# Kernel optimization log

Hardware: AMD Instinct MI355X
Metric: run time of the kernel (lower is better)

The kernel has to match this reference:

```python
import jax, jax.numpy as jnp
import numpy as np


def _next_pow2(n: int) -> int:
    return 1 << (max(int(n), 1) - 1).bit_length()


def setup_inputs() -> dict:
    key = jax.random.key(0)
    k1, k2 = jax.random.split(key)
    B, L, D, K = 8, 8192, 256, 8192
    u = jax.random.normal(k1, (B, L, D), dtype=jnp.float32)
    h = jax.random.normal(k2, (D, K), dtype=jnp.float32) * 0.02  # RandomNormal(stddev=0.02)
    return {"u": u, "h": h}


def reference(u, h):
    # Depthwise long conv via zero-padded FFT, 'same' padding.
    # Faithful to the TF code, including its h-row pairing via tf.repeat:
    # x row i (= b*D + d) is multiplied by filter row i // B.
    u = u.astype(jnp.float32)
    B, L, D = u.shape
    K = h.shape[1]
    N = _next_pow2(L + K - 1)

    x = jnp.transpose(u, (0, 2, 1)).reshape(B * D, L)      # (B*D, L)
    x_pad = jnp.pad(x, ((0, 0), (0, N - L)))               # (B*D, N)
    h_pad = jnp.pad(h, ((0, 0), (0, N - K)))               # (D, N)

    X = jnp.fft.rfft(x_pad, axis=-1)                       # (B*D, N//2+1)
    H = jnp.fft.rfft(h_pad, axis=-1)                       # (D, N//2+1)
    # tf.repeat(h, B, axis=0): repeated row i corresponds to filter i // B
    row_filter = jnp.arange(B * D) // B                    # (B*D,)
    Y = X * H[row_filter]

    y_full = jnp.fft.irfft(Y, n=N, axis=-1)                # (B*D, N)
    start = (K - 1) // 2
    y = y_full[:, start:start + L]                         # (B*D, L)
    y = y.reshape(B, D, L)
    return jnp.transpose(y, (0, 2, 1))                     # (B, L, D)
```

## Files before the change

### kernel.cpp

```cpp
#include <hip/hip_runtime.h>

#define TPB 1024

__device__ constexpr int PX(int p) { return p + 2 * (p >> 5); }

#define LDS_F2 17408
#define LDS_BYTES (LDS_F2 * 8)

#define PIF 3.14159265358979323846f
#define C8 0.92387953251128674f
#define S8 0.38268343236508978f

struct Tw { float c1,s1,c2,s2,c3,s3; };

__device__ __forceinline__ Tw tw_make(float c1, float s1) {
  Tw w;
  w.c1 = c1; w.s1 = s1;
  w.c2 = c1*c1 - s1*s1;      w.s2 = 2.f*c1*s1;
  w.c3 = c1*w.c2 - s1*w.s2;  w.s3 = c1*w.s2 + s1*w.c2;
  return w;
}
__device__ __forceinline__ Tw tw_angle(float a) {
  float s, c; __sincosf(a, &s, &c); return tw_make(c, s);
}

__device__ __forceinline__ void r4dif(float2&a,float2&b,float2&c,float2&d,const Tw&w){
  float t0r=a.x+c.x, t0i=a.y+c.y, t1r=a.x-c.x, t1i=a.y-c.y;
  float t2r=b.x+d.x, t2i=b.y+d.y, t3r=b.x-d.x, t3i=b.y-d.y;
  float u0r=t0r+t2r, u0i=t0i+t2i, u2r=t0r-t2r, u2i=t0i-t2i;
  float u1r=t1r+t3i, u1i=t1i-t3r, u3r=t1r-t3i, u3i=t1i+t3r;
  a = make_float2(u0r, u0i);
  b = make_float2(u1r*w.c1 - u1i*w.s1, u1r*w.s1 + u1i*w.c1);
  c = make_float2(u2r*w.c2 - u2i*w.s2, u2r*w.s2 + u2i*w.c2);
  d = make_float2(u3r*w.c3 - u3i*w.s3, u3r*w.s3 + u3i*w.c3);
}
__device__ __forceinline__ void r4dif_z(float2&a,float2&b,float2&c,float2&d,const Tw&w){
  float u0r=a.x+b.x, u0i=a.y+b.y, u2r=a.x-b.x, u2i=a.y-b.y;
  float u1r=a.x+b.y, u1i=a.y-b.x, u3r=a.x-b.y, u3i=a.y+b.x;
  a = make_float2(u0r, u0i);
  b = make_float2(u1r*w.c1 - u1i*w.s1, u1r*w.s1 + u1i*w.c1);
  c = make_float2(u2r*w.c2 - u2i*w.s2, u2r*w.s2 + u2i*w.c2);
  d = make_float2(u3r*w.c3 - u3i*w.s3, u3r*w.s3 + u3i*w.c3);
}
__device__ __forceinline__ void r4dif_nt(float2&a,float2&b,float2&c,float2&d){
  float t0r=a.x+c.x, t0i=a.y+c.y, t1r=a.x-c.x, t1i=a.y-c.y;
  float t2r=b.x+d.x, t2i=b.y+d.y, t3r=b.x-d.x, t3i=b.y-d.y;
  a = make_float2(t0r+t2r, t0i+t2i);
  b = make_float2(t1r+t3i, t1i-t3r);
  c = make_float2(t0r-t2r, t0i-t2i);
  d = make_float2(t1r-t3i, t1i+t3r);
}
__device__ __forceinline__ void r4dit(float2&a,float2&b,float2&c,float2&d,const Tw&w){
  float v1r=b.x*w.c1 - b.y*w.s1, v1i=b.x*w.s1 + b.y*w.c1;
  float v2r=c.x*w.c2 - c.y*w.s2, v2i=c.x*w.s2 + c.y*w.c2;
  float v3r=d.x*w.c3 - d.y*w.s3, v3i=d.x*w.s3 + d.y*w.c3;
  float ar=a.x, ai=a.y;
  a = make_float2(ar+v1r+v2r+v3r, ai+v1i+v2i+v3i);
  b = make_float2(ar-v1i-v2r+v3i, ai+v1r-v2i-v3r);
  c = make_float2(ar-v1r+v2r-v3r, ai-v1i+v2i-v3i);
  d = make_float2(ar+v1i-v2r-v3i, ai-v1r-v2i+v3r);
}
__device__ __forceinline__ void r4dit_nt(float2&a,float2&b,float2&c,float2&d){
  float v1r=b.x, v1i=b.y, v2r=c.x, v2i=c.y, v3r=d.x, v3i=d.y;
  float ar=a.x, ai=a.y;
  a = make_float2(ar+v1r+v2r+v3r, ai+v1i+v2i+v3i);
  b = make_float2(ar-v1i-v2r+v3i, ai+v1r-v2i-v3r);
  c = make_float2(ar-v1r+v2r-v3r, ai-v1i+v2i-v3i);
  d = make_float2(ar+v1i-v2r-v3i, ai-v1r-v2i+v3r);
}

__device__ __forceinline__ void r16_fwd(float2 (&e)[16], float aA, float aB) {
  float c1, s1; __sincosf(aA, &s1, &c1);
#pragma unroll
  for (int r = 0; r < 4; ++r) {
    if (r) { float t = c1*C8 + s1*S8; s1 = s1*C8 - c1*S8; c1 = t; }
    Tw w = tw_make(c1, s1);
    r4dif(e[r], e[r+4], e[r+8], e[r+12], w);
  }
  Tw wb = tw_angle(aB);
#pragma unroll
  for (int m = 0; m < 4; ++m) r4dif(e[4*m], e[4*m+1], e[4*m+2], e[4*m+3], wb);
}
__device__ __forceinline__ void r16_fwd_z(float2 (&e)[16], float aA, float aB) {
  float c1, s1; __sincosf(aA, &s1, &c1);
#pragma unroll
  for (int r = 0; r < 4; ++r) {
    if (r) { float t = c1*C8 + s1*S8; s1 = s1*C8 - c1*S8; c1 = t; }
    Tw w = tw_make(c1, s1);
    r4dif_z(e[r], e[r+4], e[r+8], e[r+12], w);
  }
  Tw wb = tw_angle(aB);
#pragma unroll
  for (int m = 0; m < 4; ++m) r4dif(e[4*m], e[4*m+1], e[4*m+2], e[4*m+3], wb);
}
__device__ __forceinline__ void r16_inv(float2 (&e)[16], float aA, float aB) {
  Tw wa = tw_angle(aA);
#pragma unroll
  for (int j = 0; j < 4; ++j) r4dit(e[4*j], e[4*j+1], e[4*j+2], e[4*j+3], wa);
  float c1, s1; __sincosf(aB, &s1, &c1);
#pragma unroll
  for (int q = 0; q < 4; ++q) {
    if (q) { float t = c1*C8 - s1*S8; s1 = s1*C8 + c1*S8; c1 = t; }
    Tw w = tw_make(c1, s1);
    r4dit(e[q], e[q+4], e[q+8], e[q+12], w);
  }
}

__device__ __forceinline__ void fwd_mid(float2* A, int tid) {
  __syncthreads();
  {
    const int c = tid & 63;
    const int pb = PX(((tid >> 6) << 10) | c);
    float2 e[16];
#pragma unroll
    for (int k = 0; k < 16; ++k) e[k] = A[pb + PX(64*k)];
    r16_fwd(e, (float)c * (-PIF/512.f), (float)c * (-PIF/128.f));
#pragma unroll
    for (int k = 0; k < 16; ++k) A[pb + PX(64*k)] = e[k];
  }
  __syncthreads();
  {
    const int c = tid & 3;
    const int pb = PX(((tid >> 2) << 6) | c);
    float2 e[16];
#pragma unroll
    for (int k = 0; k < 16; ++k) e[k] = A[pb + PX(4*k)];
    r16_fwd(e, (float)c * (-PIF/32.f), (float)c * (-PIF/8.f));
#pragma unroll
    for (int k = 0; k < 16; ++k) A[pb + PX(4*k)] = e[k];
  }
  __syncthreads();
}

__global__ __launch_bounds__(TPB) void h_fft(const float* __restrict__ h,
                                             float2* __restrict__ Hbuf) {
  extern __shared__ __align__(16) float2 A[];
  const int tid = threadIdx.x;
  const int f = blockIdx.x;
  const float* hr = h + (size_t)f * 8192;
  float2 e[16];
#pragma unroll
  for (int k = 0; k < 8; ++k) e[k] = make_float2(hr[tid + 1024*k], 0.f);
  r16_fwd_z(e, (float)tid * (-PIF/8192.f), (float)tid * (-PIF/2048.f));
  const int pt = PX(tid);
#pragma unroll
  for (int k = 0; k < 16; ++k) A[pt + PX(1024*k)] = e[k];
  fwd_mid(A, tid);
  const float sc = 1.f / 16384.f;
  float2* orow = Hbuf + (size_t)f * 16384;
  const int p4 = PX(4*tid);
#pragma unroll
  for (int m = 0; m < 4; ++m) {
    const int pp = p4 + PX(4096*m);
    float4 lo = *(const float4*)&A[pp];
    float4 hi = *(const float4*)&A[pp+2];
    float2 a = make_float2(lo.x, lo.y), b = make_float2(lo.z, lo.w);
    float2 c = make_float2(hi.x, hi.y), d = make_float2(hi.z, hi.w);
    r4dif_nt(a, b, c, d);
    const int p = 4*tid + 4096*m;
    *(float4*)&orow[p]   = make_float4(a.x*sc, a.y*sc, b.x*sc, b.y*sc);
    *(float4*)&orow[p+2] = make_float4(c.x*sc, c.y*sc, d.x*sc, d.y*sc);
  }
}

__global__ __launch_bounds__(256) void transpose_in(const float* __restrict__ u,
                                                    float* __restrict__ xT) {
  __shared__ float T[64][65];
  const int l0 = blockIdx.x * 64, d0 = blockIdx.y * 64, b = blockIdx.z;
  const int t = threadIdx.x, c = t & 15, r = t >> 4;
  const float4* u4 = (const float4*)(u + (size_t)b * 8192 * 256);
#pragma unroll
  for (int p = 0; p < 4; ++p) {
    int li = r + 16 * p;
    float4 v = u4[(size_t)(l0 + li) * 64 + (d0 >> 2) + c];
    T[4*c+0][li] = v.x; T[4*c+1][li] = v.y; T[4*c+2][li] = v.z; T[4*c+3][li] = v.w;
  }
  __syncthreads();
#pragma unroll
  for (int p = 0; p < 4; ++p) {
    int dr = r + 16 * p;
    float4 w = make_float4(T[dr][4*c+0], T[dr][4*c+1], T[dr][4*c+2], T[dr][4*c+3]);
    *(float4*)&xT[(size_t)(b * 256 + d0 + dr) * 8192 + l0 + 4 * c] = w;
  }
}

__global__ __launch_bounds__(256) void transpose_out(const float* __restrict__ yT,
                                                     float* __restrict__ out) {
  __shared__ float T[64][65];
  const int l0 = blockIdx.x * 64, d0 = blockIdx.y * 64, b = blockIdx.z;
  const int t = threadIdx.x, c = t & 15, r = t >> 4;
#pragma unroll
  for (int p = 0; p < 4; ++p) {
    int di = r + 16 * p;
    float4 v = *(const float4*)&yT[(size_t)(b * 256 + d0 + di) * 8192 + l0 + 4 * c];
    T[4*c+0][di] = v.x; T[4*c+1][di] = v.y; T[4*c+2][di] = v.z; T[4*c+3][di] = v.w;
  }
  __syncthreads();
#pragma unroll
  for (int p = 0; p < 4; ++p) {
    int lr = r + 16 * p;
    float4 w = make_float4(T[lr][4*c+0], T[lr][4*c+1], T[lr][4*c+2], T[lr][4*c+3]);
    *(float4*)&out[(size_t)(b * 8192 + l0 + lr) * 256 + d0 + 4 * c] = w;
  }
}

__global__ __launch_bounds__(TPB) void conv_main(const float* __restrict__ xT,
                                                 const float2* __restrict__ Hbuf,
                                                 float* yT) {
  extern __shared__ __align__(16) float2 A[];
  const int tid = threadIdx.x;
  const int i = blockIdx.x;
  const int f = ((i >> 5) << 3) | (i & 7);
  const int r = (f << 3) | (((i >> 3) & 3) << 1);
  const float* x0 = xT + (size_t)r * 8192;
  const float* x1 = xT + (size_t)(r + 1) * 8192;

  float2 e[16];
#pragma unroll
  for (int k = 0; k < 8; ++k)
    e[k] = make_float2(x0[tid + 1024*k], x1[tid + 1024*k]);
  const float2* Hrow = Hbuf + (size_t)f * 16384;
  float4 hpre[8];
#pragma unroll
  for (int m = 0; m < 4; ++m) {
    hpre[2*m]   = *(const float4*)&Hrow[4*tid + 4096*m];
    hpre[2*m+1] = *(const float4*)&Hrow[4*tid + 4096*m + 2];
  }
  r16_fwd_z(e, (float)tid * (-PIF/8192.f), (float)tid * (-PIF/2048.f));
  const int pt = PX(tid);
#pragma unroll
  for (int k = 0; k < 16; ++k) A[pt + PX(1024*k)] = e[k];

  fwd_mid(A, tid);

  {
    const int p4 = PX(4*tid);
#pragma unroll
    for (int m = 0; m < 4; ++m) {
      const int pp = p4 + PX(4096*m);
      float4 lo = *(const float4*)&A[pp];
      float4 hi = *(const float4*)&A[pp+2];
      float2 a = make_float2(lo.x, lo.y), b = make_float2(lo.z, lo.w);
      float2 c = make_float2(hi.x, hi.y), d = make_float2(hi.z, hi.w);
      r4dif_nt(a, b, c, d);
      float4 h0 = hpre[2*m];
      float4 h1 = hpre[2*m+1];
      float2 an = make_float2(a.x*h0.x - a.y*h0.y, a.x*h0.y + a.y*h0.x);
      float2 bn = make_float2(b.x*h0.z - b.y*h0.w, b.x*h0.w + b.y*h0.z);
      float2 cn = make_float2(c.x*h1.x - c.y*h1.y, c.x*h1.y + c.y*h1.x);
      float2 dn = make_float2(d.x*h1.z - d.y*h1.w, d.x*h1.w + d.y*h1.z);
      r4dit_nt(an, bn, cn, dn);
      *(float4*)&A[pp]   = make_float4(an.x, an.y, bn.x, bn.y);
      *(float4*)&A[pp+2] = make_float4(cn.x, cn.y, dn.x, dn.y);
    }
  }
  __syncthreads();

  {
    const int c = tid & 3;
    const int pb = PX(((tid >> 2) << 6) | c);
#pragma unroll
    for (int k = 0; k < 16; ++k) e[k] = A[pb + PX(4*k)];
    r16_inv(e, (float)c * (PIF/8.f), (float)c * (PIF/32.f));
#pragma unroll
    for (int k = 0; k < 16; ++k) A[pb + PX(4*k)] = e[k];
  }
  __syncthreads();

  {
    const int c = tid & 63;
    const int pb = PX(((tid >> 6) << 10) | c);
#pragma unroll
    for (int k = 0; k < 16; ++k) e[k] = A[pb + PX(64*k)];
    r16_inv(e, (float)c * (PIF/128.f), (float)c * (PIF/512.f));
#pragma unroll
    for (int k = 0; k < 16; ++k) A[pb + PX(64*k)] = e[k];
  }
  __syncthreads();

  {
#pragma unroll
    for (int k = 0; k < 16; ++k) e[k] = A[pt + PX(1024*k)];
    r16_inv(e, (float)tid * (PIF/2048.f), (float)tid * (PIF/8192.f));
    float* y0 = yT + (size_t)r * 8192;
    float* y1 = yT + (size_t)(r + 1) * 8192;
#pragma unroll
    for (int k = 4; k <= 10; ++k) {
      const int l = tid + 1024*k - 4095;
      y0[l] = e[k].x; y1[l] = e[k].y;
    }
    if (tid < 1023) { const int l = tid + 1024*11 - 4095; y0[l] = e[11].x; y1[l] = e[11].y; }
    else            { y0[0] = e[3].x;  y1[0] = e[3].y; }
  }
}

extern "C" void kernel_launch(void* const* d_in, const int* in_sizes, int n_in,
                              void* d_out, int out_size, void* d_ws, size_t ws_size,
                              hipStream_t stream) {
  (void)in_sizes; (void)n_in; (void)out_size; (void)ws_size;
  const float* u = (const float*)d_in[0];
  const float* h = (const float*)d_in[1];
  float* out = (float*)d_out;
  float* xT = (float*)d_ws;
  float2* Hbuf = (float2*)((char*)d_ws + (size_t)2048 * 8192 * 4);

  static_assert(LDS_BYTES == 139264, "lds");
  (void)hipFuncSetAttribute((const void*)h_fft,
      hipFuncAttributeMaxDynamicSharedMemorySize, LDS_BYTES);
  (void)hipFuncSetAttribute((const void*)conv_main,
      hipFuncAttributeMaxDynamicSharedMemorySize, LDS_BYTES);

  h_fft<<<256, TPB, LDS_BYTES, stream>>>(h, Hbuf);
  transpose_in<<<dim3(128, 4, 8), 256, 0, stream>>>(u, xT);
  conv_main<<<1024, TPB, LDS_BYTES, stream>>>(xT, Hbuf, xT);
  transpose_out<<<dim3(128, 4, 8), 256, 0, stream>>>(xT, out);
}
```

Before: 248.3 us.

## Fuse input/output transposes into the FFT convolution kernel

Removes the separate transpose_in and transpose_out kernels and the intermediate transposed workspace. conv_main now reads two adjacent channels directly from u with a stride of 256 floats, and writes float2 results directly into out. The H spectrum loads move from an up-front register prefetch to just before the pointwise multiply. This eliminates two kernel launches and a full extra round trip of the activations through global memory, at the cost of strided, poorly coalesced global accesses that rely on cache reuse across blocks.

```diff
diff --git a/kernel.cpp b/kernel.cpp
--- a/kernel.cpp
+++ b/kernel.cpp
@@ -163,69 +163,23 @@
   }
 }
 
-__global__ __launch_bounds__(256) void transpose_in(const float* __restrict__ u,
-                                                    float* __restrict__ xT) {
-  __shared__ float T[64][65];
-  const int l0 = blockIdx.x * 64, d0 = blockIdx.y * 64, b = blockIdx.z;
-  const int t = threadIdx.x, c = t & 15, r = t >> 4;
-  const float4* u4 = (const float4*)(u + (size_t)b * 8192 * 256);
-#pragma unroll
-  for (int p = 0; p < 4; ++p) {
-    int li = r + 16 * p;
-    float4 v = u4[(size_t)(l0 + li) * 64 + (d0 >> 2) + c];
-    T[4*c+0][li] = v.x; T[4*c+1][li] = v.y; T[4*c+2][li] = v.z; T[4*c+3][li] = v.w;
-  }
-  __syncthreads();
-#pragma unroll
-  for (int p = 0; p < 4; ++p) {
-    int dr = r + 16 * p;
-    float4 w = make_float4(T[dr][4*c+0], T[dr][4*c+1], T[dr][4*c+2], T[dr][4*c+3]);
-    *(float4*)&xT[(size_t)(b * 256 + d0 + dr) * 8192 + l0 + 4 * c] = w;
-  }
-}
-
-__global__ __launch_bounds__(256) void transpose_out(const float* __restrict__ yT,
-                                                     float* __restrict__ out) {
-  __shared__ float T[64][65];
-  const int l0 = blockIdx.x * 64, d0 = blockIdx.y * 64, b = blockIdx.z;
-  const int t = threadIdx.x, c = t & 15, r = t >> 4;
-#pragma unroll
-  for (int p = 0; p < 4; ++p) {
-    int di = r + 16 * p;
-    float4 v = *(const float4*)&yT[(size_t)(b * 256 + d0 + di) * 8192 + l0 + 4 * c];
-    T[4*c+0][di] = v.x; T[4*c+1][di] = v.y; T[4*c+2][di] = v.z; T[4*c+3][di] = v.w;
-  }
-  __syncthreads();
-#pragma unroll
-  for (int p = 0; p < 4; ++p) {
-    int lr = r + 16 * p;
-    float4 w = make_float4(T[lr][4*c+0], T[lr][4*c+1], T[lr][4*c+2], T[lr][4*c+3]);
-    *(float4*)&out[(size_t)(b * 8192 + l0 + lr) * 256 + d0 + 4 * c] = w;
-  }
-}
-
-__global__ __launch_bounds__(TPB) void conv_main(const float* __restrict__ xT,
+__global__ __launch_bounds__(TPB) void conv_main(const float* __restrict__ u,
                                                  const float2* __restrict__ Hbuf,
-                                                 float* yT) {
+                                                 float* __restrict__ out) {
   extern __shared__ __align__(16) float2 A[];
   const int tid = threadIdx.x;
   const int i = blockIdx.x;
-  const int f = ((i >> 5) << 3) | (i & 7);
-  const int r = (f << 3) | (((i >> 3) & 3) << 1);
-  const float* x0 = xT + (size_t)r * 8192;
-  const float* x1 = xT + (size_t)(r + 1) * 8192;
+  const int X = i & 7, q = i >> 8, m = (i >> 3) & 31;
+  const int combo = q * 8 + X;
+  const int b = combo >> 2, s = combo & 3;
+  const int d = s * 64 + 2 * m;
+  const int f = (b * 256 + d) >> 3;
+  const float* ub = u + (size_t)b * 8192 * 256 + d;
 
   float2 e[16];
 #pragma unroll
   for (int k = 0; k < 8; ++k)
-    e[k] = make_float2(x0[tid + 1024*k], x1[tid + 1024*k]);
-  const float2* Hrow = Hbuf + (size_t)f * 16384;
-  float4 hpre[8];
-#pragma unroll
-  for (int m = 0; m < 4; ++m) {
-    hpre[2*m]   = *(const float4*)&Hrow[4*tid + 4096*m];
-    hpre[2*m+1] = *(const float4*)&Hrow[4*tid + 4096*m + 2];
-  }
+    e[k] = *(const float2*)&ub[(size_t)(tid + 1024 * k) * 256];
   r16_fwd_z(e, (float)tid * (-PIF/8192.f), (float)tid * (-PIF/2048.f));
   const int pt = PX(tid);
 #pragma unroll
@@ -234,21 +188,23 @@
   fwd_mid(A, tid);
 
   {
+    const float2* Hrow = Hbuf + (size_t)f * 16384;
     const int p4 = PX(4*tid);
 #pragma unroll
-    for (int m = 0; m < 4; ++m) {
-      const int pp = p4 + PX(4096*m);
+    for (int mm = 0; mm < 4; ++mm) {
+      const int pp = p4 + PX(4096*mm);
       float4 lo = *(const float4*)&A[pp];
       float4 hi = *(const float4*)&A[pp+2];
-      float2 a = make_float2(lo.x, lo.y), b = make_float2(lo.z, lo.w);
-      float2 c = make_float2(hi.x, hi.y), d = make_float2(hi.z, hi.w);
-      r4dif_nt(a, b, c, d);
-      float4 h0 = hpre[2*m];
-      float4 h1 = hpre[2*m+1];
+      float2 a = make_float2(lo.x, lo.y), b2 = make_float2(lo.z, lo.w);
+      float2 c = make_float2(hi.x, hi.y), d2 = make_float2(hi.z, hi.w);
+      r4dif_nt(a, b2, c, d2);
+      const int p = 4*tid + 4096*mm;
+      float4 h0 = *(const float4*)&Hrow[p];
+      float4 h1 = *(const float4*)&Hrow[p+2];
       float2 an = make_float2(a.x*h0.x - a.y*h0.y, a.x*h0.y + a.y*h0.x);
-      float2 bn = make_float2(b.x*h0.z - b.y*h0.w, b.x*h0.w + b.y*h0.z);
+      float2 bn = make_float2(b2.x*h0.z - b2.y*h0.w, b2.x*h0.w + b2.y*h0.z);
       float2 cn = make_float2(c.x*h1.x - c.y*h1.y, c.x*h1.y + c.y*h1.x);
-      float2 dn = make_float2(d.x*h1.z - d.y*h1.w, d.x*h1.w + d.y*h1.z);
+      float2 dn = make_float2(d2.x*h1.z - d2.y*h1.w, d2.x*h1.w + d2.y*h1.z);
       r4dit_nt(an, bn, cn, dn);
       *(float4*)&A[pp]   = make_float4(an.x, an.y, bn.x, bn.y);
       *(float4*)&A[pp+2] = make_float4(cn.x, cn.y, dn.x, dn.y);
@@ -282,15 +238,14 @@
 #pragma unroll
     for (int k = 0; k < 16; ++k) e[k] = A[pt + PX(1024*k)];
     r16_inv(e, (float)tid * (PIF/2048.f), (float)tid * (PIF/8192.f));
-    float* y0 = yT + (size_t)r * 8192;
-    float* y1 = yT + (size_t)(r + 1) * 8192;
+    float2* ob = (float2*)(out + (size_t)b * 8192 * 256 + d);
 #pragma unroll
     for (int k = 4; k <= 10; ++k) {
       const int l = tid + 1024*k - 4095;
-      y0[l] = e[k].x; y1[l] = e[k].y;
+      ob[(size_t)l * 128] = e[k];
     }
-    if (tid < 1023) { const int l = tid + 1024*11 - 4095; y0[l] = e[11].x; y1[l] = e[11].y; }
-    else            { y0[0] = e[3].x;  y1[0] = e[3].y; }
+    if (tid < 1023) { const int l = tid + 1024*11 - 4095; ob[(size_t)l * 128] = e[11]; }
+    else            { ob[0] = e[3]; }
   }
 }
 
@@ -301,8 +256,7 @@
   const float* u = (const float*)d_in[0];
   const float* h = (const float*)d_in[1];
   float* out = (float*)d_out;
-  float* xT = (float*)d_ws;
-  float2* Hbuf = (float2*)((char*)d_ws + (size_t)2048 * 8192 * 4);
+  float2* Hbuf = (float2*)d_ws;
 
   static_assert(LDS_BYTES == 139264, "lds");
   (void)hipFuncSetAttribute((const void*)h_fft,
@@ -311,7 +265,5 @@
       hipFuncAttributeMaxDynamicSharedMemorySize, LDS_BYTES);
 
   h_fft<<<256, TPB, LDS_BYTES, stream>>>(h, Hbuf);
-  transpose_in<<<dim3(128, 4, 8), 256, 0, stream>>>(u, xT);
-  conv_main<<<1024, TPB, LDS_BYTES, stream>>>(xT, Hbuf, xT);
-  transpose_out<<<dim3(128, 4, 8), 256, 0, stream>>>(xT, out);
-}
+  conv_main<<<1024, TPB, LDS_BYTES, stream>>>(u, Hbuf, out);
+}
```

After: 278.2 us. +12.0%, slower.
